# Kernel optimization log

Measured on AMD Instinct MI355X. Metric: run time of the kernel, lower is better.

## Reference

```python
import jax, jax.numpy as jnp
import numpy as np

B, T, I = 64, 256, 512
H, C = 1024, 1024
S_CTX = 256


def setup_inputs() -> dict:
    key = jax.random.key(0)
    ks = jax.random.split(key, 20)
    stdv = 1.0 / np.sqrt(H)
    stdv_c = 1.0 / np.sqrt(C)
    u = lambda k, shape, s: jax.random.uniform(k, shape, jnp.float32, -s, s)
    return {
        "input": jax.random.normal(ks[0], (B, T, I), jnp.float32),
        "hx": jax.random.normal(ks[1], (B, H), jnp.float32),
        "cx": jax.random.normal(ks[2], (B, H), jnp.float32),
        "ctx": jax.random.normal(ks[3], (S_CTX, B, C), jnp.float32),
        "iw1": u(ks[4], (4 * H, I), stdv),
        "hw1": u(ks[5], (4 * H, H), stdv),
        "ib1": jnp.zeros((4 * H,), jnp.float32),
        "hb1": jnp.zeros((4 * H,), jnp.float32),
        "iw2": u(ks[6], (4 * H, C), stdv_c),
        "hw2": u(ks[7], (4 * H, H), stdv),
        "ib2": jnp.zeros((4 * H,), jnp.float32),
        "hb2": jnp.zeros((4 * H,), jnp.float32),
        "c2a": u(ks[8], (C, C), stdv_c),
        "b_c2a": jnp.zeros((C,), jnp.float32),
        "h2a": u(ks[9], (C, H), stdv_c),
        "i2a": u(ks[10], (I, C), stdv_c),
        "r2a": u(ks[11], (C, 1), stdv_c),
    }


def _lstm_gates(gates, c_prev):
    i, f, g, o = jnp.split(gates, 4, axis=1)
    c = jax.nn.sigmoid(f) * c_prev + jax.nn.sigmoid(i) * jnp.tanh(g)
    h = jax.nn.sigmoid(o) * jnp.tanh(c)
    return h, c


def reference(input, hx, cx, ctx, iw1, hw1, ib1, hb1, iw2, hw2, ib2, hb2,
              c2a, b_c2a, h2a, i2a, r2a):
    x = jnp.transpose(input, (1, 0, 2))                      # (T, B, I)
    projected_ctx = ctx @ c2a + b_c2a                        # (S, B, C)
    projected_input = x @ i2a                                # (T, B, C)
    r = r2a[:, 0]                                            # (C,)

    def step(carry, xs):
        hx, cx = carry
        x_t, pi_t = xs
        gates = x_t @ iw1.T + ib1 + hx @ hw1.T + hb1
        hy, cy = _lstm_gates(gates, cx)
        hidden_ctx = hy @ h2a.T                              # (B, C)
        s = jnp.tanh(projected_ctx + hidden_ctx[None] + pi_t[None])  # (S,B,C)
        alpha = jax.nn.softmax(jnp.einsum('sbc,c->bs', s, r), axis=-1)
        wctx = jnp.einsum('sbc,bs->bc', ctx, alpha)          # (B, C)
        gates2 = wctx @ iw2.T + ib2 + hy @ hw2.T + hb2
        hy2, cy2 = _lstm_gates(gates2, cy)
        return (hy2, cy2), hy2

    (h_f, c_f), output = jax.lax.scan(step, (hx, cx), (x, projected_input))
    return output, h_f, c_f  # output: (T, B, H)
```

## Files before the change

### kernel.cpp

```cpp
#include <hip/hip_runtime.h>

typedef __attribute__((ext_vector_type(8))) short short8v;
typedef __attribute__((ext_vector_type(4))) float f32x4;

#define MFMA(a,b,c) __builtin_amdgcn_mfma_f32_16x16x32_bf16((a),(b),(c),0,0,0)

__device__ __forceinline__ float rcpf_(float x){ return __builtin_amdgcn_rcpf(x); }
__device__ __forceinline__ float sigf(float x){ return rcpf_(1.0f + __expf(-x)); }
__device__ __forceinline__ float tanhfast(float x){ return fmaf(-2.0f, rcpf_(1.0f + __expf(2.0f*x)), 1.0f); }
__device__ __forceinline__ float bf2f(unsigned short u){ union{unsigned int i; float f;} v; v.i = ((unsigned int)u)<<16; return v.f; }
__device__ __forceinline__ float u2f(unsigned int i){ union{unsigned int i; float f;} v; v.i = i; return v.f; }
__device__ __forceinline__ unsigned short f2bf(float f){ union{float f; unsigned int i;} v; v.f=f; unsigned int x = v.i + 0x7fffu + ((v.i>>16)&1u); return (unsigned short)(x>>16); }
__device__ __forceinline__ float4 ld4(const float* p){ return *(const float4*)p; }

__global__ __launch_bounds__(256) void k_w1(const float* __restrict__ iw1, const float* __restrict__ hw1,
                                            ushort* __restrict__ w1b){
  int idx4 = (blockIdx.x*256 + threadIdx.x) * 4;
  int n = idx4 / 1536, k = idx4 % 1536;
  float4 v = (k < 512) ? *(const float4*)(iw1 + n*512 + k)
                       : *(const float4*)(hw1 + n*1024 + (k - 512));
  ushort4 o; o.x=f2bf(v.x); o.y=f2bf(v.y); o.z=f2bf(v.z); o.w=f2bf(v.w);
  *(ushort4*)(w1b + idx4) = o;
}
__global__ __launch_bounds__(256) void k_w2(const float* __restrict__ h2a, const float* __restrict__ hw2,
                                            ushort* __restrict__ w2b){
  int idx4 = (blockIdx.x*256 + threadIdx.x) * 4;
  int n = idx4 >> 10, k = idx4 & 1023;
  float4 v = (n < 1024) ? *(const float4*)(h2a + n*1024 + k)
                        : *(const float4*)(hw2 + (n-1024)*1024 + k);
  ushort4 o; o.x=f2bf(v.x); o.y=f2bf(v.y); o.z=f2bf(v.z); o.w=f2bf(v.w);
  *(ushort4*)(w2b + idx4) = o;
}
__global__ __launch_bounds__(256) void k_w3(const float* __restrict__ iw2, ushort* __restrict__ w3b){
  int idx4 = (blockIdx.x*256 + threadIdx.x) * 4;
  float4 v = *(const float4*)(iw2 + idx4);
  ushort4 o; o.x=f2bf(v.x); o.y=f2bf(v.y); o.z=f2bf(v.z); o.w=f2bf(v.w);
  *(ushort4*)(w3b + idx4) = o;
}
__global__ __launch_bounds__(256) void k_ctxT(const float* __restrict__ ctx, ushort* __restrict__ ctxb){
  int idx4 = (blockIdx.x*256 + threadIdx.x) * 4;
  int c = idx4 & 1023, s = (idx4 >> 10) & 255, b = idx4 >> 18;
  float4 v = *(const float4*)(ctx + (s*64 + b)*1024 + c);
  ushort4 o; o.x=f2bf(v.x); o.y=f2bf(v.y); o.z=f2bf(v.z); o.w=f2bf(v.w);
  *(ushort4*)(ctxb + idx4) = o;
}
__global__ __launch_bounds__(256) void k_xb(const float* __restrict__ inp, ushort* __restrict__ xb){
  int idx4 = (blockIdx.x*256 + threadIdx.x) * 4;
  int k = idx4 & 511, b = (idx4 >> 9) & 63, t = idx4 >> 15;
  float4 v = *(const float4*)(inp + (b*256 + t)*512 + k);
  ushort4 o; o.x=f2bf(v.x); o.y=f2bf(v.y); o.z=f2bf(v.z); o.w=f2bf(v.w);
  *(ushort4*)(xb + idx4) = o;
}
__global__ __launch_bounds__(256) void k_i2aT(const float* __restrict__ i2a, ushort* __restrict__ i2aT){
  int idx = blockIdx.x*256 + threadIdx.x;
  int n = idx & 1023, k = idx >> 10;
  i2aT[n*512 + k] = f2bf(i2a[k*1024 + n]);
}
__global__ __launch_bounds__(256) void k_cvthx(const float* __restrict__ hx, ushort* __restrict__ hxbbf){
  int i4 = (blockIdx.x*256 + threadIdx.x)*4;
  float4 v = ld4(hx + i4);
  ushort4 o; o.x=f2bf(v.x); o.y=f2bf(v.y); o.z=f2bf(v.z); o.w=f2bf(v.w);
  *(ushort4*)(hxbbf + i4) = o;
}

__global__ __launch_bounds__(256) void k_pc(const float* __restrict__ ctxp, const float* __restrict__ c2a,
                                            const float* __restrict__ bc, ushort* __restrict__ pcb){
  __shared__ __align__(16) float As[32][68];
  __shared__ __align__(16) float Bs[32][68];
  const int tid = threadIdx.x;
  const int m0 = blockIdx.x * 64;
  const int n0 = blockIdx.y * 64;
  const int tx = tid & 15, ty = tid >> 4;
  float acc[4][4] = {};
  for (int k0 = 0; k0 < 1024; k0 += 32){
#pragma unroll
    for (int l = 0; l < 8; ++l){
      int idx = l*256 + tid; int m = idx >> 5, k = idx & 31;
      As[k][m] = ctxp[(m0+m)*1024 + k0 + k];
    }
#pragma unroll
    for (int l = 0; l < 8; ++l){
      int idx = l*256 + tid; int k = idx >> 6, n = idx & 63;
      Bs[k][n] = c2a[(k0+k)*1024 + n0 + n];
    }
    __syncthreads();
#pragma unroll
    for (int k = 0; k < 32; ++k){
      float4 a4 = *(const float4*)&As[k][4*ty];
      float4 b4 = *(const float4*)&Bs[k][4*tx];
      float av[4] = {a4.x, a4.y, a4.z, a4.w};
      float bv[4] = {b4.x, b4.y, b4.z, b4.w};
#pragma unroll
      for (int i = 0; i < 4; ++i)
#pragma unroll
        for (int j = 0; j < 4; ++j) acc[i][j] = fmaf(av[i], bv[j], acc[i][j]);
    }
    __syncthreads();
  }
#pragma unroll
  for (int i = 0; i < 4; ++i){
    int m = m0 + 4*ty + i;
    int n = n0 + 4*tx;
    ushort4 o;
    o.x = f2bf(acc[i][0] + bc[n]);
    o.y = f2bf(acc[i][1] + bc[n+1]);
    o.z = f2bf(acc[i][2] + bc[n+2]);
    o.w = f2bf(acc[i][3] + bc[n+3]);
    *(ushort4*)(pcb + m*1024 + n) = o;
  }
}

__global__ __launch_bounds__(128) void k_gates1(const ushort* __restrict__ xb, const ushort* __restrict__ hxbf,
                                                const ushort* __restrict__ w1b, float* __restrict__ g1p, int t){
  const int lane = threadIdx.x & 63;
  const int w = threadIdx.x >> 6;
  const int kh = blockIdx.y;
  const int ncol = blockIdx.x*32 + w*16 + (lane & 15);
  const int ko = (lane >> 4) << 3;
  const int row = lane & 15;
  const ushort* wp = w1b + ncol*1536 + kh*768 + ko;
  f32x4 a0 = {0.f,0.f,0.f,0.f}, a1 = a0, a2 = a0, a3 = a0;
  if (kh == 0){
    const ushort* xp = xb + (t*64 + row)*512 + ko;
#pragma unroll
    for (int it = 0; it < 16; ++it){
      short8v bf = *(const short8v*)(wp + it*32);
      short8v x0 = *(const short8v*)(xp + it*32);
      short8v x1 = *(const short8v*)(xp + it*32 + 16*512);
      short8v x2 = *(const short8v*)(xp + it*32 + 32*512);
      short8v x3 = *(const short8v*)(xp + it*32 + 48*512);
      a0 = MFMA(x0, bf, a0); a1 = MFMA(x1, bf, a1); a2 = MFMA(x2, bf, a2); a3 = MFMA(x3, bf, a3);
    }
    const ushort* hp = hxbf + row*1024 + ko;
#pragma unroll
    for (int it = 0; it < 8; ++it){
      short8v bf = *(const short8v*)(wp + (16+it)*32);
      short8v x0 = *(const short8v*)(hp + it*32);
      short8v x1 = *(const short8v*)(hp + it*32 + 16*1024);
      short8v x2 = *(const short8v*)(hp + it*32 + 32*1024);
      short8v x3 = *(const short8v*)(hp + it*32 + 48*1024);
      a0 = MFMA(x0, bf, a0); a1 = MFMA(x1, bf, a1); a2 = MFMA(x2, bf, a2); a3 = MFMA(x3, bf, a3);
    }
  } else {
    const ushort* hp = hxbf + row*1024 + 256 + ko;
#pragma unroll
    for (int it = 0; it < 24; ++it){
      short8v bf = *(const short8v*)(wp + it*32);
      short8v x0 = *(const short8v*)(hp + it*32);
      short8v x1 = *(const short8v*)(hp + it*32 + 16*1024);
      short8v x2 = *(const short8v*)(hp + it*32 + 32*1024);
      short8v x3 = *(const short8v*)(hp + it*32 + 48*1024);
      a0 = MFMA(x0, bf, a0); a1 = MFMA(x1, bf, a1); a2 = MFMA(x2, bf, a2); a3 = MFMA(x3, bf, a3);
    }
  }
  float* op = g1p + kh*(64*4096) + ncol;
  const int mb = (lane >> 4) * 4;
#pragma unroll
  for (int r = 0; r < 4; ++r){
    op[(mb + r)*4096]      = a0[r];
    op[(16 + mb + r)*4096] = a1[r];
    op[(32 + mb + r)*4096] = a2[r];
    op[(48 + mb + r)*4096] = a3[r];
  }
}

__global__ __launch_bounds__(128) void k_hyproj(const ushort* __restrict__ hybf, const ushort* __restrict__ w2b,
                                                const ushort* __restrict__ xb, const ushort* __restrict__ i2aT,
                                                float* __restrict__ hyp, int t){
  const int lane = threadIdx.x & 63;
  const int w = threadIdx.x >> 6;
  const int kh = blockIdx.y;
  const int ncol = blockIdx.x*32 + w*16 + (lane & 15);
  const int ko = (lane >> 4) << 3;
  const int row = lane & 15;
  const ushort* wp = w2b + ncol*1024 + kh*512 + ko;
  const ushort* hp = hybf + row*1024 + kh*512 + ko;
  f32x4 a0 = {0.f,0.f,0.f,0.f}, a1 = a0, a2 = a0, a3 = a0;
#pragma unroll
  for (int it = 0; it < 16; ++it){
    short8v bf = *(const short8v*)(wp + it*32);
    short8v x0 = *(const short8v*)(hp + it*32);
    short8v x1 = *(const short8v*)(hp + it*32 + 16*1024);
    short8v x2 = *(const short8v*)(hp + it*32 + 32*1024);
    short8v x3 = *(const short8v*)(hp + it*32 + 48*1024);
    a0 = MFMA(x0, bf, a0); a1 = MFMA(x1, bf, a1); a2 = MFMA(x2, bf, a2); a3 = MFMA(x3, bf, a3);
  }
  if (kh == 1 && ncol < 1024){
    const ushort* ip = i2aT + ncol*512 + ko;
    const ushort* xp = xb + (t*64 + row)*512 + ko;
#pragma unroll
    for (int it = 0; it < 16; ++it){
      short8v bf = *(const short8v*)(ip + it*32);
      short8v x0 = *(const short8v*)(xp + it*32);
      short8v x1 = *(const short8v*)(xp + it*32 + 16*512);
      short8v x2 = *(const short8v*)(xp + it*32 + 32*512);
      short8v x3 = *(const short8v*)(xp + it*32 + 48*512);
      a0 = MFMA(x0, bf, a0); a1 = MFMA(x1, bf, a1); a2 = MFMA(x2, bf, a2); a3 = MFMA(x3, bf, a3);
    }
  }
  float* op = hyp + kh*(64*5120) + ncol;
  const int mb = (lane >> 4) * 4;
#pragma unroll
  for (int r = 0; r < 4; ++r){
    op[(mb + r)*5120]      = a0[r];
    op[(16 + mb + r)*5120] = a1[r];
    op[(32 + mb + r)*5120] = a2[r];
    op[(48 + mb + r)*5120] = a3[r];
  }
}

__global__ __launch_bounds__(128) void k_gates2(const ushort* __restrict__ wctxbf, const ushort* __restrict__ w3b,
                                                float* __restrict__ g2p){
  const int lane = threadIdx.x & 63;
  const int w = threadIdx.x >> 6;
  const int kh = blockIdx.y;
  const int ncol = blockIdx.x*32 + w*16 + (lane & 15);
  const int ko = (lane >> 4) << 3;
  const int row = lane & 15;
  const ushort* wp = w3b + ncol*1024 + kh*512 + ko;
  const ushort* ap = wctxbf + row*1024 + kh*512 + ko;
  f32x4 a0 = {0.f,0.f,0.f,0.f}, a1 = a0, a2 = a0, a3 = a0;
#pragma unroll
  for (int it = 0; it < 16; ++it){
    short8v bf = *(const short8v*)(wp + it*32);
    short8v x0 = *(const short8v*)(ap + it*32);
    short8v x1 = *(const short8v*)(ap + it*32 + 16*1024);
    short8v x2 = *(const short8v*)(ap + it*32 + 32*1024);
    short8v x3 = *(const short8v*)(ap + it*32 + 48*1024);
    a0 = MFMA(x0, bf, a0); a1 = MFMA(x1, bf, a1); a2 = MFMA(x2, bf, a2); a3 = MFMA(x3, bf, a3);
  }
  float* op = g2p + kh*(64*4096) + ncol;
  const int mb = (lane >> 4) * 4;
#pragma unroll
  for (int r = 0; r < 4; ++r){
    op[(mb + r)*4096]      = a0[r];
    op[(16 + mb + r)*4096] = a1[r];
    op[(32 + mb + r)*4096] = a2[r];
    op[(48 + mb + r)*4096] = a3[r];
  }
}

__global__ __launch_bounds__(256) void k_lstm1(const float* __restrict__ g1p, const float* __restrict__ cxb,
                                               const float* __restrict__ ib1, const float* __restrict__ hb1,
                                               float* __restrict__ cym, ushort* __restrict__ hybf){
  int i4 = (blockIdx.x*256 + threadIdx.x)*4;
  int b = i4 >> 10, h = i4 & 1023;
  const float* p0 = g1p + b*4096;
  const float* p1 = g1p + 64*4096 + b*4096;
#define LOADG1(off) ({ float4 A=ld4(p0+(off)); float4 Bv=ld4(p1+(off)); float4 C=ld4(ib1+(off)); float4 D=ld4(hb1+(off)); \
                       make_float4(A.x+Bv.x+C.x+D.x, A.y+Bv.y+C.y+D.y, A.z+Bv.z+C.z+D.z, A.w+Bv.w+C.w+D.w); })
  float4 gi = LOADG1(h);
  float4 gf = LOADG1(h+1024);
  float4 gg = LOADG1(h+2048);
  float4 go = LOADG1(h+3072);
#undef LOADG1
  float4 cx4 = ld4(cxb + i4);
  float c0 = sigf(gf.x)*cx4.x + sigf(gi.x)*tanhfast(gg.x);
  float c1 = sigf(gf.y)*cx4.y + sigf(gi.y)*tanhfast(gg.y);
  float c2 = sigf(gf.z)*cx4.z + sigf(gi.z)*tanhfast(gg.z);
  float c3 = sigf(gf.w)*cx4.w + sigf(gi.w)*tanhfast(gg.w);
  *(float4*)(cym + i4) = make_float4(c0,c1,c2,c3);
  ushort4 o;
  o.x = f2bf(sigf(go.x)*tanhfast(c0));
  o.y = f2bf(sigf(go.y)*tanhfast(c1));
  o.z = f2bf(sigf(go.z)*tanhfast(c2));
  o.w = f2bf(sigf(go.w)*tanhfast(c3));
  *(ushort4*)(hybf + i4) = o;
}

__global__ __launch_bounds__(256) void k_lstm2(const float* __restrict__ g2p, const float* __restrict__ hyp,
                                               const float* __restrict__ cym,
                                               const float* __restrict__ ib2, const float* __restrict__ hb2,
                                               float* __restrict__ out, float* __restrict__ hxb,
                                               ushort* __restrict__ hxbbf, float* __restrict__ cxb, int t){
  int i4 = (blockIdx.x*256 + threadIdx.x)*4;
  int b = i4 >> 10, h = i4 & 1023;
  const float* p0 = g2p + b*4096;
  const float* p1 = g2p + 64*4096 + b*4096;
  const float* q0 = hyp + b*5120 + 1024;
  const float* q1 = hyp + 64*5120 + b*5120 + 1024;
#define LOADG2(off) ({ float4 A=ld4(p0+(off)); float4 Bv=ld4(p1+(off)); float4 C=ld4(q0+(off)); float4 D=ld4(q1+(off)); \
                       float4 E=ld4(ib2+(off)); float4 F=ld4(hb2+(off)); \
                       make_float4(A.x+Bv.x+C.x+D.x+E.x+F.x, A.y+Bv.y+C.y+D.y+E.y+F.y, \
                                   A.z+Bv.z+C.z+D.z+E.z+F.z, A.w+Bv.w+C.w+D.w+E.w+F.w); })
  float4 gi = LOADG2(h);
  float4 gf = LOADG2(h+1024);
  float4 gg = LOADG2(h+2048);
  float4 go = LOADG2(h+3072);
#undef LOADG2
  float4 cm4 = ld4(cym + i4);
  float c0 = sigf(gf.x)*cm4.x + sigf(gi.x)*tanhfast(gg.x);
  float c1 = sigf(gf.y)*cm4.y + sigf(gi.y)*tanhfast(gg.y);
  float c2 = sigf(gf.z)*cm4.z + sigf(gi.z)*tanhfast(gg.z);
  float c3 = sigf(gf.w)*cm4.w + sigf(gi.w)*tanhfast(gg.w);
  float h0 = sigf(go.x)*tanhfast(c0);
  float h1 = sigf(go.y)*tanhfast(c1);
  float h2 = sigf(go.z)*tanhfast(c2);
  float h3 = sigf(go.w)*tanhfast(c3);
  float4 h4 = make_float4(h0,h1,h2,h3);
  *(float4*)(out + t*65536 + i4) = h4;
  *(float4*)(hxb + i4) = h4;
  *(float4*)(cxb + i4) = make_float4(c0,c1,c2,c3);
  ushort4 o; o.x=f2bf(h0); o.y=f2bf(h1); o.z=f2bf(h2); o.w=f2bf(h3);
  *(ushort4*)(hxbbf + i4) = o;
}

__global__ __launch_bounds__(256) void k_logits(const ushort* __restrict__ pcb, const float* __restrict__ hyp,
                                                const float* __restrict__ r2a, float* __restrict__ logits){
  const int w = threadIdx.x >> 6, lane = threadIdx.x & 63;
  const int p = blockIdx.x*4 + w;
  const int s = p >> 6, b = p & 63;
  const ushort* pp = pcb + (s*64 + b)*1024;
  const float* q0 = hyp + b*5120;
  const float* q1 = hyp + 64*5120 + b*5120;
  float acc = 0.0f;
#pragma unroll
  for (int half = 0; half < 2; ++half){
    int cb = lane*8 + half*512;
    uint4 pv = *(const uint4*)(pp + cb);
    float4 qa0 = ld4(q0+cb), qa1 = ld4(q0+cb+4);
    float4 qb0 = ld4(q1+cb), qb1 = ld4(q1+cb+4);
    float4 r0 = ld4(r2a+cb), r1 = ld4(r2a+cb+4);
    acc = fmaf(tanhfast(u2f(pv.x << 16)         + qa0.x + qb0.x), r0.x, acc);
    acc = fmaf(tanhfast(u2f(pv.x & 0xffff0000u) + qa0.y + qb0.y), r0.y, acc);
    acc = fmaf(tanhfast(u2f(pv.y << 16)         + qa0.z + qb0.z), r0.z, acc);
    acc = fmaf(tanhfast(u2f(pv.y & 0xffff0000u) + qa0.w + qb0.w), r0.w, acc);
    acc = fmaf(tanhfast(u2f(pv.z << 16)         + qa1.x + qb1.x), r1.x, acc);
    acc = fmaf(tanhfast(u2f(pv.z & 0xffff0000u) + qa1.y + qb1.y), r1.y, acc);
    acc = fmaf(tanhfast(u2f(pv.w << 16)         + qa1.z + qb1.z), r1.z, acc);
    acc = fmaf(tanhfast(u2f(pv.w & 0xffff0000u) + qa1.w + qb1.w), r1.w, acc);
  }
#pragma unroll
  for (int off = 32; off; off >>= 1) acc += __shfl_xor(acc, off);
  if (lane == 0) logits[b*256 + s] = acc;
}

__global__ __launch_bounds__(256) void k_attnout(const float* __restrict__ logits, const ushort* __restrict__ ctxb,
                                                 float* __restrict__ partial){
  __shared__ float red[256];
  __shared__ float sm[256];
  __shared__ float al[32];
  const int bi = blockIdx.x >> 3, ch = blockIdx.x & 7;
  const int tid = threadIdx.x;
  float l = logits[bi*256 + tid];
  red[tid] = l; __syncthreads();
  for (int s = 128; s; s >>= 1){ if (tid < s) red[tid] = fmaxf(red[tid], red[tid+s]); __syncthreads(); }
  float mx = red[0]; __syncthreads();
  float e = __expf(l - mx);
  sm[tid] = e; red[tid] = e; __syncthreads();
  for (int s = 128; s; s >>= 1){ if (tid < s) red[tid] += red[tid+s]; __syncthreads(); }
  float inv = rcpf_(red[0]);
  if (tid < 32) al[tid] = sm[ch*32 + tid] * inv;
  __syncthreads();
  const int c0 = tid * 4;
  const ushort* cp = ctxb + (bi*256 + ch*32)*1024 + c0;
  float a0=0.f, a1=0.f, a2=0.f, a3=0.f;
#pragma unroll 4
  for (int s = 0; s < 32; ++s){
    ushort4 v = *(const ushort4*)(cp + s*1024);
    float aw = al[s];
    a0 = fmaf(aw, bf2f(v.x), a0);
    a1 = fmaf(aw, bf2f(v.y), a1);
    a2 = fmaf(aw, bf2f(v.z), a2);
    a3 = fmaf(aw, bf2f(v.w), a3);
  }
  float4 o; o.x=a0; o.y=a1; o.z=a2; o.w=a3;
  *(float4*)(partial + (ch*64 + bi)*1024 + c0) = o;
}

__global__ __launch_bounds__(256) void k_wctxred(const float* __restrict__ partial, ushort* __restrict__ wctxbf){
  int i4 = (blockIdx.x*256 + threadIdx.x) * 4;
  float4 s = *(const float4*)(partial + i4);
#pragma unroll
  for (int ch = 1; ch < 8; ++ch){
    float4 v = *(const float4*)(partial + ch*65536 + i4);
    s.x += v.x; s.y += v.y; s.z += v.z; s.w += v.w;
  }
  ushort4 o; o.x=f2bf(s.x); o.y=f2bf(s.y); o.z=f2bf(s.z); o.w=f2bf(s.w);
  *(ushort4*)(wctxbf + i4) = o;
}

extern "C" void kernel_launch(void* const* d_in, const int* in_sizes, int n_in,
                              void* d_out, int out_size, void* d_ws, size_t ws_size,
                              hipStream_t stream) {
  const float* input = (const float*)d_in[0];
  const float* hx    = (const float*)d_in[1];
  const float* cx    = (const float*)d_in[2];
  const float* ctxp  = (const float*)d_in[3];
  const float* iw1   = (const float*)d_in[4];
  const float* hw1   = (const float*)d_in[5];
  const float* ib1   = (const float*)d_in[6];
  const float* hb1   = (const float*)d_in[7];
  const float* iw2   = (const float*)d_in[8];
  const float* hw2   = (const float*)d_in[9];
  const float* ib2   = (const float*)d_in[10];
  const float* hb2   = (const float*)d_in[11];
  const float* c2a   = (const float*)d_in[12];
  const float* b_c2a = (const float*)d_in[13];
  const float* h2a   = (const float*)d_in[14];
  const float* i2a   = (const float*)d_in[15];
  const float* r2a   = (const float*)d_in[16];
  float* out = (float*)d_out;

  char* base = (char*)d_ws;
  ushort* pcb    = (ushort*)(base);
  ushort* ctxb   = (ushort*)(base + 33554432);
  ushort* xb     = (ushort*)(base + 67108864);
  ushort* w1b    = (ushort*)(base + 83886080);
  ushort* w2b    = (ushort*)(base + 96468992);
  ushort* w3b    = (ushort*)(base + 106954752);
  ushort* i2aT   = (ushort*)(base + 115343360);
  float*  g1p    = (float*)(base + 116391936);
  float*  hyp    = (float*)(base + 118489088);
  float*  g2p    = (float*)(base + 121110528);
  float*  cym    = (float*)(base + 123207680);
  float*  hxb    = (float*)(base + 123469824);
  float*  cxb    = (float*)(base + 123731968);
  ushort* hybf   = (ushort*)(base + 123994112);
  ushort* hxbbf  = (ushort*)(base + 124125184);
  ushort* wctxbf = (ushort*)(base + 124256256);
  float*  logits = (float*)(base + 124387328);
  float*  partial= (float*)(base + 124452864);

  hipMemcpyAsync(hxb, hx, 262144, hipMemcpyDeviceToDevice, stream);
  hipMemcpyAsync(cxb, cx, 262144, hipMemcpyDeviceToDevice, stream);

  k_cvthx<<<64,   256, 0, stream>>>(hx, hxbbf);
  k_w1  <<<6144,  256, 0, stream>>>(iw1, hw1, w1b);
  k_w2  <<<5120,  256, 0, stream>>>(h2a, hw2, w2b);
  k_w3  <<<4096,  256, 0, stream>>>(iw2, w3b);
  k_ctxT<<<16384, 256, 0, stream>>>(ctxp, ctxb);
  k_xb  <<<8192,  256, 0, stream>>>(input, xb);
  k_i2aT<<<2048,  256, 0, stream>>>(i2a, i2aT);
  k_pc  <<<dim3(256,16), 256, 0, stream>>>(ctxp, c2a, b_c2a, pcb);

  for (int t = 0; t < 256; ++t){
    k_gates1 <<<dim3(128,2), 128, 0, stream>>>(xb, hxbbf, w1b, g1p, t);
    k_lstm1  <<<64,  256, 0, stream>>>(g1p, cxb, ib1, hb1, cym, hybf);
    k_hyproj <<<dim3(160,2), 128, 0, stream>>>(hybf, w2b, xb, i2aT, hyp, t);
    k_logits <<<4096,256, 0, stream>>>(pcb, hyp, r2a, logits);
    k_attnout<<<512, 256, 0, stream>>>(logits, ctxb, partial);
    k_wctxred<<<64,  256, 0, stream>>>(partial, wctxbf);
    k_gates2 <<<dim3(128,2), 128, 0, stream>>>(wctxbf, w3b, g2p);
    k_lstm2  <<<64,  256, 0, stream>>>(g2p, hyp, cym, ib2, hb2, out, hxb, hxbbf, cxb, t);
  }

  hipMemcpyAsync(out + 16777216,         hxb, 262144, hipMemcpyDeviceToDevice, stream);
  hipMemcpyAsync(out + 16777216 + 65536, cxb, 262144, hipMemcpyDeviceToDevice, stream);
}
```

Before: 16.23 ms.

## Fuse per-step gate GEMMs with LSTM cells and drop split-K partial buffers

Merges the gate GEMM and LSTM elementwise kernels into one kernel per layer: the four gate groups and two K halves are computed by eight waves and reduced through shared memory. The hidden projection drops the K split and tiles over batch strips instead, so the partial-sum buffer goes away. Attention output now does the full context sum per block, which removes the separate reduction kernel. Logits blocks keep the query and r vectors in registers across many source positions. Per-step launches fall from eight to five and global round trips for partial sums are removed, but the fused kernels run only 64 blocks, which lowers parallelism.

```diff
diff --git a/kernel.cpp b/kernel.cpp
--- a/kernel.cpp
+++ b/kernel.cpp
@@ -110,274 +110,235 @@
   }
 }
 
-__global__ __launch_bounds__(128) void k_gates1(const ushort* __restrict__ xb, const ushort* __restrict__ hxbf,
-                                                const ushort* __restrict__ w1b, float* __restrict__ g1p, int t){
-  const int lane = threadIdx.x & 63;
-  const int w = threadIdx.x >> 6;
-  const int kh = blockIdx.y;
-  const int ncol = blockIdx.x*32 + w*16 + (lane & 15);
+__global__ __launch_bounds__(512) void k_step1(const ushort* __restrict__ xb, const ushort* __restrict__ hxbf,
+                                               const ushort* __restrict__ w1b,
+                                               const float* __restrict__ ib1, const float* __restrict__ hb1,
+                                               const float* __restrict__ cxb,
+                                               float* __restrict__ cym, ushort* __restrict__ hybf, int t){
+  __shared__ float lds[2][4][64][17];
+  const int tid = threadIdx.x;
+  const int lane = tid & 63;
+  const int w = tid >> 6;
+  const int g = w & 3;
+  const int kh = w >> 2;
+  const int j = blockIdx.x;
+  const int ncol = g*1024 + j*16 + (lane & 15);
   const int ko = (lane >> 4) << 3;
-  const int row = lane & 15;
+  const int arow = lane & 15;
   const ushort* wp = w1b + ncol*1536 + kh*768 + ko;
   f32x4 a0 = {0.f,0.f,0.f,0.f}, a1 = a0, a2 = a0, a3 = a0;
   if (kh == 0){
-    const ushort* xp = xb + (t*64 + row)*512 + ko;
+    const ushort* xp = xb + (t*64 + arow)*512 + ko;
 #pragma unroll
     for (int it = 0; it < 16; ++it){
       short8v bf = *(const short8v*)(wp + it*32);
-      short8v x0 = *(const short8v*)(xp + it*32);
-      short8v x1 = *(const short8v*)(xp + it*32 + 16*512);
-      short8v x2 = *(const short8v*)(xp + it*32 + 32*512);
-      short8v x3 = *(const short8v*)(xp + it*32 + 48*512);
-      a0 = MFMA(x0, bf, a0); a1 = MFMA(x1, bf, a1); a2 = MFMA(x2, bf, a2); a3 = MFMA(x3, bf, a3);
-    }
-    const ushort* hp = hxbf + row*1024 + ko;
+      a0 = MFMA(*(const short8v*)(xp + it*32), bf, a0);
+      a1 = MFMA(*(const short8v*)(xp + it*32 + 16*512), bf, a1);
+      a2 = MFMA(*(const short8v*)(xp + it*32 + 32*512), bf, a2);
+      a3 = MFMA(*(const short8v*)(xp + it*32 + 48*512), bf, a3);
+    }
+    const ushort* hp = hxbf + arow*1024 + ko;
 #pragma unroll
     for (int it = 0; it < 8; ++it){
       short8v bf = *(const short8v*)(wp + (16+it)*32);
-      short8v x0 = *(const short8v*)(hp + it*32);
-      short8v x1 = *(const short8v*)(hp + it*32 + 16*1024);
-      short8v x2 = *(const short8v*)(hp + it*32 + 32*1024);
-      short8v x3 = *(const short8v*)(hp + it*32 + 48*1024);
-      a0 = MFMA(x0, bf, a0); a1 = MFMA(x1, bf, a1); a2 = MFMA(x2, bf, a2); a3 = MFMA(x3, bf, a3);
+      a0 = MFMA(*(const short8v*)(hp + it*32), bf, a0);
+      a1 = MFMA(*(const short8v*)(hp + it*32 + 16*1024), bf, a1);
+      a2 = MFMA(*(const short8v*)(hp + it*32 + 32*1024), bf, a2);
+      a3 = MFMA(*(const short8v*)(hp + it*32 + 48*1024), bf, a3);
     }
   } else {
-    const ushort* hp = hxbf + row*1024 + 256 + ko;
+    const ushort* hp = hxbf + arow*1024 + 256 + ko;
 #pragma unroll
     for (int it = 0; it < 24; ++it){
       short8v bf = *(const short8v*)(wp + it*32);
-      short8v x0 = *(const short8v*)(hp + it*32);
-      short8v x1 = *(const short8v*)(hp + it*32 + 16*1024);
-      short8v x2 = *(const short8v*)(hp + it*32 + 32*1024);
-      short8v x3 = *(const short8v*)(hp + it*32 + 48*1024);
-      a0 = MFMA(x0, bf, a0); a1 = MFMA(x1, bf, a1); a2 = MFMA(x2, bf, a2); a3 = MFMA(x3, bf, a3);
-    }
-  }
-  float* op = g1p + kh*(64*4096) + ncol;
-  const int mb = (lane >> 4) * 4;
-#pragma unroll
-  for (int r = 0; r < 4; ++r){
-    op[(mb + r)*4096]      = a0[r];
-    op[(16 + mb + r)*4096] = a1[r];
-    op[(32 + mb + r)*4096] = a2[r];
-    op[(48 + mb + r)*4096] = a3[r];
-  }
-}
-
-__global__ __launch_bounds__(128) void k_hyproj(const ushort* __restrict__ hybf, const ushort* __restrict__ w2b,
+      a0 = MFMA(*(const short8v*)(hp + it*32), bf, a0);
+      a1 = MFMA(*(const short8v*)(hp + it*32 + 16*1024), bf, a1);
+      a2 = MFMA(*(const short8v*)(hp + it*32 + 32*1024), bf, a2);
+      a3 = MFMA(*(const short8v*)(hp + it*32 + 48*1024), bf, a3);
+    }
+  }
+  {
+    const int ccol = lane & 15;
+    const int rb = (lane >> 4) * 4;
+#pragma unroll
+    for (int r = 0; r < 4; ++r){
+      lds[kh][g][rb + r][ccol]      = a0[r];
+      lds[kh][g][16 + rb + r][ccol] = a1[r];
+      lds[kh][g][32 + rb + r][ccol] = a2[r];
+      lds[kh][g][48 + rb + r][ccol] = a3[r];
+    }
+  }
+  __syncthreads();
+  const int e = tid * 2;
+  const int row = e >> 4;
+  const int c0 = e & 15;
+  const int h = j*16 + c0;
+#pragma unroll
+  for (int u = 0; u < 2; ++u){
+    int c = c0 + u, hh = h + u;
+    float gi = lds[0][0][row][c] + lds[1][0][row][c] + ib1[hh]        + hb1[hh];
+    float gf = lds[0][1][row][c] + lds[1][1][row][c] + ib1[1024+hh]   + hb1[1024+hh];
+    float gg = lds[0][2][row][c] + lds[1][2][row][c] + ib1[2048+hh]   + hb1[2048+hh];
+    float go = lds[0][3][row][c] + lds[1][3][row][c] + ib1[3072+hh]   + hb1[3072+hh];
+    float cc = sigf(gf)*cxb[row*1024 + hh] + sigf(gi)*tanhfast(gg);
+    cym[row*1024 + hh] = cc;
+    hybf[row*1024 + hh] = f2bf(sigf(go)*tanhfast(cc));
+  }
+}
+
+__global__ __launch_bounds__(256) void k_hyproj(const ushort* __restrict__ hybf, const ushort* __restrict__ w2b,
                                                 const ushort* __restrict__ xb, const ushort* __restrict__ i2aT,
                                                 float* __restrict__ hyp, int t){
   const int lane = threadIdx.x & 63;
-  const int w = threadIdx.x >> 6;
-  const int kh = blockIdx.y;
-  const int ncol = blockIdx.x*32 + w*16 + (lane & 15);
+  const int strip = threadIdx.x >> 6;
+  const int ntile = blockIdx.x * 16;
+  const int ncol = ntile + (lane & 15);
   const int ko = (lane >> 4) << 3;
-  const int row = lane & 15;
-  const ushort* wp = w2b + ncol*1024 + kh*512 + ko;
-  const ushort* hp = hybf + row*1024 + kh*512 + ko;
-  f32x4 a0 = {0.f,0.f,0.f,0.f}, a1 = a0, a2 = a0, a3 = a0;
-#pragma unroll
-  for (int it = 0; it < 16; ++it){
-    short8v bf = *(const short8v*)(wp + it*32);
-    short8v x0 = *(const short8v*)(hp + it*32);
-    short8v x1 = *(const short8v*)(hp + it*32 + 16*1024);
-    short8v x2 = *(const short8v*)(hp + it*32 + 32*1024);
-    short8v x3 = *(const short8v*)(hp + it*32 + 48*1024);
-    a0 = MFMA(x0, bf, a0); a1 = MFMA(x1, bf, a1); a2 = MFMA(x2, bf, a2); a3 = MFMA(x3, bf, a3);
-  }
-  if (kh == 1 && ncol < 1024){
+  const int arow = strip*16 + (lane & 15);
+  const ushort* wp = w2b + ncol*1024 + ko;
+  const ushort* hp = hybf + arow*1024 + ko;
+  f32x4 acc = {0.f,0.f,0.f,0.f};
+#pragma unroll
+  for (int it = 0; it < 32; ++it)
+    acc = MFMA(*(const short8v*)(hp + it*32), *(const short8v*)(wp + it*32), acc);
+  if (ntile < 1024){
     const ushort* ip = i2aT + ncol*512 + ko;
-    const ushort* xp = xb + (t*64 + row)*512 + ko;
-#pragma unroll
-    for (int it = 0; it < 16; ++it){
-      short8v bf = *(const short8v*)(ip + it*32);
-      short8v x0 = *(const short8v*)(xp + it*32);
-      short8v x1 = *(const short8v*)(xp + it*32 + 16*512);
-      short8v x2 = *(const short8v*)(xp + it*32 + 32*512);
-      short8v x3 = *(const short8v*)(xp + it*32 + 48*512);
-      a0 = MFMA(x0, bf, a0); a1 = MFMA(x1, bf, a1); a2 = MFMA(x2, bf, a2); a3 = MFMA(x3, bf, a3);
-    }
-  }
-  float* op = hyp + kh*(64*5120) + ncol;
-  const int mb = (lane >> 4) * 4;
-#pragma unroll
-  for (int r = 0; r < 4; ++r){
-    op[(mb + r)*5120]      = a0[r];
-    op[(16 + mb + r)*5120] = a1[r];
-    op[(32 + mb + r)*5120] = a2[r];
-    op[(48 + mb + r)*5120] = a3[r];
-  }
-}
-
-__global__ __launch_bounds__(128) void k_gates2(const ushort* __restrict__ wctxbf, const ushort* __restrict__ w3b,
-                                                float* __restrict__ g2p){
-  const int lane = threadIdx.x & 63;
-  const int w = threadIdx.x >> 6;
-  const int kh = blockIdx.y;
-  const int ncol = blockIdx.x*32 + w*16 + (lane & 15);
-  const int ko = (lane >> 4) << 3;
-  const int row = lane & 15;
-  const ushort* wp = w3b + ncol*1024 + kh*512 + ko;
-  const ushort* ap = wctxbf + row*1024 + kh*512 + ko;
-  f32x4 a0 = {0.f,0.f,0.f,0.f}, a1 = a0, a2 = a0, a3 = a0;
-#pragma unroll
-  for (int it = 0; it < 16; ++it){
-    short8v bf = *(const short8v*)(wp + it*32);
-    short8v x0 = *(const short8v*)(ap + it*32);
-    short8v x1 = *(const short8v*)(ap + it*32 + 16*1024);
-    short8v x2 = *(const short8v*)(ap + it*32 + 32*1024);
-    short8v x3 = *(const short8v*)(ap + it*32 + 48*1024);
-    a0 = MFMA(x0, bf, a0); a1 = MFMA(x1, bf, a1); a2 = MFMA(x2, bf, a2); a3 = MFMA(x3, bf, a3);
-  }
-  float* op = g2p + kh*(64*4096) + ncol;
-  const int mb = (lane >> 4) * 4;
-#pragma unroll
-  for (int r = 0; r < 4; ++r){
-    op[(mb + r)*4096]      = a0[r];
-    op[(16 + mb + r)*4096] = a1[r];
-    op[(32 + mb + r)*4096] = a2[r];
-    op[(48 + mb + r)*4096] = a3[r];
-  }
-}
-
-__global__ __launch_bounds__(256) void k_lstm1(const float* __restrict__ g1p, const float* __restrict__ cxb,
-                                               const float* __restrict__ ib1, const float* __restrict__ hb1,
-                                               float* __restrict__ cym, ushort* __restrict__ hybf){
-  int i4 = (blockIdx.x*256 + threadIdx.x)*4;
-  int b = i4 >> 10, h = i4 & 1023;
-  const float* p0 = g1p + b*4096;
-  const float* p1 = g1p + 64*4096 + b*4096;
-#define LOADG1(off) ({ float4 A=ld4(p0+(off)); float4 Bv=ld4(p1+(off)); float4 C=ld4(ib1+(off)); float4 D=ld4(hb1+(off)); \
-                       make_float4(A.x+Bv.x+C.x+D.x, A.y+Bv.y+C.y+D.y, A.z+Bv.z+C.z+D.z, A.w+Bv.w+C.w+D.w); })
-  float4 gi = LOADG1(h);
-  float4 gf = LOADG1(h+1024);
-  float4 gg = LOADG1(h+2048);
-  float4 go = LOADG1(h+3072);
-#undef LOADG1
-  float4 cx4 = ld4(cxb + i4);
-  float c0 = sigf(gf.x)*cx4.x + sigf(gi.x)*tanhfast(gg.x);
-  float c1 = sigf(gf.y)*cx4.y + sigf(gi.y)*tanhfast(gg.y);
-  float c2 = sigf(gf.z)*cx4.z + sigf(gi.z)*tanhfast(gg.z);
-  float c3 = sigf(gf.w)*cx4.w + sigf(gi.w)*tanhfast(gg.w);
-  *(float4*)(cym + i4) = make_float4(c0,c1,c2,c3);
-  ushort4 o;
-  o.x = f2bf(sigf(go.x)*tanhfast(c0));
-  o.y = f2bf(sigf(go.y)*tanhfast(c1));
-  o.z = f2bf(sigf(go.z)*tanhfast(c2));
-  o.w = f2bf(sigf(go.w)*tanhfast(c3));
-  *(ushort4*)(hybf + i4) = o;
-}
-
-__global__ __launch_bounds__(256) void k_lstm2(const float* __restrict__ g2p, const float* __restrict__ hyp,
-                                               const float* __restrict__ cym,
-                                               const float* __restrict__ ib2, const float* __restrict__ hb2,
-                                               float* __restrict__ out, float* __restrict__ hxb,
-                                               ushort* __restrict__ hxbbf, float* __restrict__ cxb, int t){
-  int i4 = (blockIdx.x*256 + threadIdx.x)*4;
-  int b = i4 >> 10, h = i4 & 1023;
-  const float* p0 = g2p + b*4096;
-  const float* p1 = g2p + 64*4096 + b*4096;
-  const float* q0 = hyp + b*5120 + 1024;
-  const float* q1 = hyp + 64*5120 + b*5120 + 1024;
-#define LOADG2(off) ({ float4 A=ld4(p0+(off)); float4 Bv=ld4(p1+(off)); float4 C=ld4(q0+(off)); float4 D=ld4(q1+(off)); \
-                       float4 E=ld4(ib2+(off)); float4 F=ld4(hb2+(off)); \
-                       make_float4(A.x+Bv.x+C.x+D.x+E.x+F.x, A.y+Bv.y+C.y+D.y+E.y+F.y, \
-                                   A.z+Bv.z+C.z+D.z+E.z+F.z, A.w+Bv.w+C.w+D.w+E.w+F.w); })
-  float4 gi = LOADG2(h);
-  float4 gf = LOADG2(h+1024);
-  float4 gg = LOADG2(h+2048);
-  float4 go = LOADG2(h+3072);
-#undef LOADG2
-  float4 cm4 = ld4(cym + i4);
-  float c0 = sigf(gf.x)*cm4.x + sigf(gi.x)*tanhfast(gg.x);
-  float c1 = sigf(gf.y)*cm4.y + sigf(gi.y)*tanhfast(gg.y);
-  float c2 = sigf(gf.z)*cm4.z + sigf(gi.z)*tanhfast(gg.z);
-  float c3 = sigf(gf.w)*cm4.w + sigf(gi.w)*tanhfast(gg.w);
-  float h0 = sigf(go.x)*tanhfast(c0);
-  float h1 = sigf(go.y)*tanhfast(c1);
-  float h2 = sigf(go.z)*tanhfast(c2);
-  float h3 = sigf(go.w)*tanhfast(c3);
-  float4 h4 = make_float4(h0,h1,h2,h3);
-  *(float4*)(out + t*65536 + i4) = h4;
-  *(float4*)(hxb + i4) = h4;
-  *(float4*)(cxb + i4) = make_float4(c0,c1,c2,c3);
-  ushort4 o; o.x=f2bf(h0); o.y=f2bf(h1); o.z=f2bf(h2); o.w=f2bf(h3);
-  *(ushort4*)(hxbbf + i4) = o;
+    const ushort* xp = xb + (t*64 + arow)*512 + ko;
+#pragma unroll
+    for (int it = 0; it < 16; ++it)
+      acc = MFMA(*(const short8v*)(xp + it*32), *(const short8v*)(ip + it*32), acc);
+  }
+  float* op = hyp + ncol;
+  const int rb = strip*16 + (lane >> 4)*4;
+#pragma unroll
+  for (int r = 0; r < 4; ++r) op[(rb + r)*5120] = acc[r];
 }
 
 __global__ __launch_bounds__(256) void k_logits(const ushort* __restrict__ pcb, const float* __restrict__ hyp,
                                                 const float* __restrict__ r2a, float* __restrict__ logits){
+  const int b = blockIdx.x >> 2;
+  const int sq = blockIdx.x & 3;
   const int w = threadIdx.x >> 6, lane = threadIdx.x & 63;
-  const int p = blockIdx.x*4 + w;
-  const int s = p >> 6, b = p & 63;
-  const ushort* pp = pcb + (s*64 + b)*1024;
-  const float* q0 = hyp + b*5120;
-  const float* q1 = hyp + 64*5120 + b*5120;
-  float acc = 0.0f;
-#pragma unroll
-  for (int half = 0; half < 2; ++half){
-    int cb = lane*8 + half*512;
-    uint4 pv = *(const uint4*)(pp + cb);
-    float4 qa0 = ld4(q0+cb), qa1 = ld4(q0+cb+4);
-    float4 qb0 = ld4(q1+cb), qb1 = ld4(q1+cb+4);
-    float4 r0 = ld4(r2a+cb), r1 = ld4(r2a+cb+4);
-    acc = fmaf(tanhfast(u2f(pv.x << 16)         + qa0.x + qb0.x), r0.x, acc);
-    acc = fmaf(tanhfast(u2f(pv.x & 0xffff0000u) + qa0.y + qb0.y), r0.y, acc);
-    acc = fmaf(tanhfast(u2f(pv.y << 16)         + qa0.z + qb0.z), r0.z, acc);
-    acc = fmaf(tanhfast(u2f(pv.y & 0xffff0000u) + qa0.w + qb0.w), r0.w, acc);
-    acc = fmaf(tanhfast(u2f(pv.z << 16)         + qa1.x + qb1.x), r1.x, acc);
-    acc = fmaf(tanhfast(u2f(pv.z & 0xffff0000u) + qa1.y + qb1.y), r1.y, acc);
-    acc = fmaf(tanhfast(u2f(pv.w << 16)         + qa1.z + qb1.z), r1.z, acc);
-    acc = fmaf(tanhfast(u2f(pv.w & 0xffff0000u) + qa1.w + qb1.w), r1.w, acc);
-  }
-#pragma unroll
-  for (int off = 32; off; off >>= 1) acc += __shfl_xor(acc, off);
-  if (lane == 0) logits[b*256 + s] = acc;
+  const float* qp = hyp + b*5120 + lane*16;
+  const float* rp = r2a + lane*16;
+  float q[16], r[16];
+#pragma unroll
+  for (int i = 0; i < 4; ++i){
+    float4 qv = ld4(qp + i*4);
+    float4 rv = ld4(rp + i*4);
+    q[4*i]=qv.x; q[4*i+1]=qv.y; q[4*i+2]=qv.z; q[4*i+3]=qv.w;
+    r[4*i]=rv.x; r[4*i+1]=rv.y; r[4*i+2]=rv.z; r[4*i+3]=rv.w;
+  }
+#pragma unroll 4
+  for (int pi = 0; pi < 16; ++pi){
+    const int s = sq*64 + w*16 + pi;
+    const ushort* pp = pcb + (s*64 + b)*1024 + lane*16;
+    uint4 v0 = *(const uint4*)pp;
+    uint4 v1 = *(const uint4*)(pp + 8);
+    float acc;
+    acc  = tanhfast(u2f(v0.x << 16)         + q[0])  * r[0];
+    acc  = fmaf(tanhfast(u2f(v0.x & 0xffff0000u) + q[1]),  r[1],  acc);
+    acc  = fmaf(tanhfast(u2f(v0.y << 16)         + q[2]),  r[2],  acc);
+    acc  = fmaf(tanhfast(u2f(v0.y & 0xffff0000u) + q[3]),  r[3],  acc);
+    acc  = fmaf(tanhfast(u2f(v0.z << 16)         + q[4]),  r[4],  acc);
+    acc  = fmaf(tanhfast(u2f(v0.z & 0xffff0000u) + q[5]),  r[5],  acc);
+    acc  = fmaf(tanhfast(u2f(v0.w << 16)         + q[6]),  r[6],  acc);
+    acc  = fmaf(tanhfast(u2f(v0.w & 0xffff0000u) + q[7]),  r[7],  acc);
+    acc  = fmaf(tanhfast(u2f(v1.x << 16)         + q[8]),  r[8],  acc);
+    acc  = fmaf(tanhfast(u2f(v1.x & 0xffff0000u) + q[9]),  r[9],  acc);
+    acc  = fmaf(tanhfast(u2f(v1.y << 16)         + q[10]), r[10], acc);
+    acc  = fmaf(tanhfast(u2f(v1.y & 0xffff0000u) + q[11]), r[11], acc);
+    acc  = fmaf(tanhfast(u2f(v1.z << 16)         + q[12]), r[12], acc);
+    acc  = fmaf(tanhfast(u2f(v1.z & 0xffff0000u) + q[13]), r[13], acc);
+    acc  = fmaf(tanhfast(u2f(v1.w << 16)         + q[14]), r[14], acc);
+    acc  = fmaf(tanhfast(u2f(v1.w & 0xffff0000u) + q[15]), r[15], acc);
+#pragma unroll
+    for (int off = 32; off; off >>= 1) acc += __shfl_xor(acc, off);
+    if (lane == 0) logits[b*256 + s] = acc;
+  }
 }
 
 __global__ __launch_bounds__(256) void k_attnout(const float* __restrict__ logits, const ushort* __restrict__ ctxb,
-                                                 float* __restrict__ partial){
+                                                 ushort* __restrict__ wctxbf){
   __shared__ float red[256];
-  __shared__ float sm[256];
-  __shared__ float al[32];
-  const int bi = blockIdx.x >> 3, ch = blockIdx.x & 7;
+  __shared__ float al[256];
+  const int bi = blockIdx.x >> 2, cq = blockIdx.x & 3;
   const int tid = threadIdx.x;
   float l = logits[bi*256 + tid];
   red[tid] = l; __syncthreads();
   for (int s = 128; s; s >>= 1){ if (tid < s) red[tid] = fmaxf(red[tid], red[tid+s]); __syncthreads(); }
   float mx = red[0]; __syncthreads();
   float e = __expf(l - mx);
-  sm[tid] = e; red[tid] = e; __syncthreads();
+  al[tid] = e; red[tid] = e; __syncthreads();
   for (int s = 128; s; s >>= 1){ if (tid < s) red[tid] += red[tid+s]; __syncthreads(); }
   float inv = rcpf_(red[0]);
-  if (tid < 32) al[tid] = sm[ch*32 + tid] * inv;
+  const int c = cq*256 + tid;
+  const ushort* cp = ctxb + bi*256*1024 + c;
+  float acc = 0.0f;
+#pragma unroll 8
+  for (int s = 0; s < 256; ++s)
+    acc = fmaf(al[s], bf2f(cp[s*1024]), acc);
+  wctxbf[bi*1024 + c] = f2bf(acc * inv);
+}
+
+__global__ __launch_bounds__(512) void k_step2(const ushort* __restrict__ wctxbf, const ushort* __restrict__ w3b,
+                                               const float* __restrict__ hyp,
+                                               const float* __restrict__ ib2, const float* __restrict__ hb2,
+                                               const float* __restrict__ cym,
+                                               float* __restrict__ out, float* __restrict__ hxb,
+                                               ushort* __restrict__ hxbbf, float* __restrict__ cxb, int t){
+  __shared__ float lds[2][4][64][17];
+  const int tid = threadIdx.x;
+  const int lane = tid & 63;
+  const int w = tid >> 6;
+  const int g = w & 3;
+  const int kh = w >> 2;
+  const int j = blockIdx.x;
+  const int ncol = g*1024 + j*16 + (lane & 15);
+  const int ko = (lane >> 4) << 3;
+  const int arow = lane & 15;
+  const ushort* wp = w3b + ncol*1024 + kh*512 + ko;
+  const ushort* ap = wctxbf + arow*1024 + kh*512 + ko;
+  f32x4 a0 = {0.f,0.f,0.f,0.f}, a1 = a0, a2 = a0, a3 = a0;
+#pragma unroll
+  for (int it = 0; it < 16; ++it){
+    short8v bf = *(const short8v*)(wp + it*32);
+    a0 = MFMA(*(const short8v*)(ap + it*32), bf, a0);
+    a1 = MFMA(*(const short8v*)(ap + it*32 + 16*1024), bf, a1);
+    a2 = MFMA(*(const short8v*)(ap + it*32 + 32*1024), bf, a2);
+    a3 = MFMA(*(const short8v*)(ap + it*32 + 48*1024), bf, a3);
+  }
+  {
+    const int ccol = lane & 15;
+    const int rb = (lane >> 4) * 4;
+#pragma unroll
+    for (int r = 0; r < 4; ++r){
+      lds[kh][g][rb + r][ccol]      = a0[r];
+      lds[kh][g][16 + rb + r][ccol] = a1[r];
+      lds[kh][g][32 + rb + r][ccol] = a2[r];
+      lds[kh][g][48 + rb + r][ccol] = a3[r];
+    }
+  }
   __syncthreads();
-  const int c0 = tid * 4;
-  const ushort* cp = ctxb + (bi*256 + ch*32)*1024 + c0;
-  float a0=0.f, a1=0.f, a2=0.f, a3=0.f;
-#pragma unroll 4
-  for (int s = 0; s < 32; ++s){
-    ushort4 v = *(const ushort4*)(cp + s*1024);
-    float aw = al[s];
-    a0 = fmaf(aw, bf2f(v.x), a0);
-    a1 = fmaf(aw, bf2f(v.y), a1);
-    a2 = fmaf(aw, bf2f(v.z), a2);
-    a3 = fmaf(aw, bf2f(v.w), a3);
-  }
-  float4 o; o.x=a0; o.y=a1; o.z=a2; o.w=a3;
-  *(float4*)(partial + (ch*64 + bi)*1024 + c0) = o;
-}
-
-__global__ __launch_bounds__(256) void k_wctxred(const float* __restrict__ partial, ushort* __restrict__ wctxbf){
-  int i4 = (blockIdx.x*256 + threadIdx.x) * 4;
-  float4 s = *(const float4*)(partial + i4);
-#pragma unroll
-  for (int ch = 1; ch < 8; ++ch){
-    float4 v = *(const float4*)(partial + ch*65536 + i4);
-    s.x += v.x; s.y += v.y; s.z += v.z; s.w += v.w;
-  }
-  ushort4 o; o.x=f2bf(s.x); o.y=f2bf(s.y); o.z=f2bf(s.z); o.w=f2bf(s.w);
-  *(ushort4*)(wctxbf + i4) = o;
+  const int e = tid * 2;
+  const int row = e >> 4;
+  const int c0 = e & 15;
+#pragma unroll
+  for (int u = 0; u < 2; ++u){
+    int c = c0 + u;
+    int hh = j*16 + c;
+    const float* g2 = hyp + row*5120 + 1024;
+    float gi = lds[0][0][row][c] + lds[1][0][row][c] + g2[hh]        + ib2[hh]      + hb2[hh];
+    float gf = lds[0][1][row][c] + lds[1][1][row][c] + g2[1024+hh]   + ib2[1024+hh] + hb2[1024+hh];
+    float gg = lds[0][2][row][c] + lds[1][2][row][c] + g2[2048+hh]   + ib2[2048+hh] + hb2[2048+hh];
+    float go = lds[0][3][row][c] + lds[1][3][row][c] + g2[3072+hh]   + ib2[3072+hh] + hb2[3072+hh];
+    float cc = sigf(gf)*cym[row*1024 + hh] + sigf(gi)*tanhfast(gg);
+    float hv = sigf(go)*tanhfast(cc);
+    out[t*65536 + row*1024 + hh] = hv;
+    hxb[row*1024 + hh] = hv;
+    cxb[row*1024 + hh] = cc;
+    hxbbf[row*1024 + hh] = f2bf(hv);
+  }
 }
 
 extern "C" void kernel_launch(void* const* d_in, const int* in_sizes, int n_in,
@@ -410,17 +371,14 @@
   ushort* w2b    = (ushort*)(base + 96468992);
   ushort* w3b    = (ushort*)(base + 106954752);
   ushort* i2aT   = (ushort*)(base + 115343360);
-  float*  g1p    = (float*)(base + 116391936);
-  float*  hyp    = (float*)(base + 118489088);
-  float*  g2p    = (float*)(base + 121110528);
-  float*  cym    = (float*)(base + 123207680);
-  float*  hxb    = (float*)(base + 123469824);
-  float*  cxb    = (float*)(base + 123731968);
-  ushort* hybf   = (ushort*)(base + 123994112);
-  ushort* hxbbf  = (ushort*)(base + 124125184);
-  ushort* wctxbf = (ushort*)(base + 124256256);
-  float*  logits = (float*)(base + 124387328);
-  float*  partial= (float*)(base + 124452864);
+  float*  hyp    = (float*)(base + 116391936);
+  float*  cym    = (float*)(base + 117702656);
+  float*  hxb    = (float*)(base + 117964800);
+  float*  cxb    = (float*)(base + 118226944);
+  ushort* hybf   = (ushort*)(base + 118489088);
+  ushort* hxbbf  = (ushort*)(base + 118620160);
+  ushort* wctxbf = (ushort*)(base + 118751232);
+  float*  logits = (float*)(base + 118882304);
 
   hipMemcpyAsync(hxb, hx, 262144, hipMemcpyDeviceToDevice, stream);
   hipMemcpyAsync(cxb, cx, 262144, hipMemcpyDeviceToDevice, stream);
@@ -435,14 +393,11 @@
   k_pc  <<<dim3(256,16), 256, 0, stream>>>(ctxp, c2a, b_c2a, pcb);
 
   for (int t = 0; t < 256; ++t){
-    k_gates1 <<<dim3(128,2), 128, 0, stream>>>(xb, hxbbf, w1b, g1p, t);
-    k_lstm1  <<<64,  256, 0, stream>>>(g1p, cxb, ib1, hb1, cym, hybf);
-    k_hyproj <<<dim3(160,2), 128, 0, stream>>>(hybf, w2b, xb, i2aT, hyp, t);
-    k_logits <<<4096,256, 0, stream>>>(pcb, hyp, r2a, logits);
-    k_attnout<<<512, 256, 0, stream>>>(logits, ctxb, partial);
-    k_wctxred<<<64,  256, 0, stream>>>(partial, wctxbf);
-    k_gates2 <<<dim3(128,2), 128, 0, stream>>>(wctxbf, w3b, g2p);
-    k_lstm2  <<<64,  256, 0, stream>>>(g2p, hyp, cym, ib2, hb2, out, hxb, hxbbf, cxb, t);
+    k_step1  <<<64,  512, 0, stream>>>(xb, hxbbf, w1b, ib1, hb1, cxb, cym, hybf, t);
+    k_hyproj <<<320, 256, 0, stream>>>(hybf, w2b, xb, i2aT, hyp, t);
+    k_logits <<<256, 256, 0, stream>>>(pcb, hyp, r2a, logits);
+    k_attnout<<<256, 256, 0, stream>>>(logits, ctxb, wctxbf);
+    k_step2  <<<64,  512, 0, stream>>>(wctxbf, w3b, hyp, ib2, hb2, cym, out, hxb, hxbbf, cxb, t);
   }
 
   hipMemcpyAsync(out + 16777216,         hxb, 262144, hipMemcpyDeviceToDevice, stream);
```

Result: slower. 26.24 ms (+61.7%).
